# Performance work log

Hardware: AMD Instinct MI355X
Metric: run time of the kernel (lower is better)

## Reference

```python
import jax, jax.numpy as jnp
import numpy as np


def setup_inputs() -> dict:
    key = jax.random.key(0)
    k1, k2 = jax.random.split(key)
    B, N, D = 256, 50000, 2048
    queries = jax.random.normal(k1, (B, D), dtype=jnp.float32)
    bank = jax.random.normal(k2, (N, D), dtype=jnp.float32)
    return {"queries": queries, "bank": bank}


def reference(queries, bank):
    # Cosine similarity of every query against every bank row, fused as one
    # GEMM + row-norm scaling (original repeats the query N times per item
    # in a Python loop; math is identical).
    eps = jnp.float32(1e-12)
    q_norm = jnp.sqrt(jnp.sum(queries * queries, axis=1, keepdims=True))  # [B,1]
    b_norm = jnp.sqrt(jnp.sum(bank * bank, axis=1))                       # [N]
    dots = jnp.einsum('bd,nd->bn', queries, bank)                         # [B,N]
    scores = dots / jnp.maximum(q_norm * b_norm[None, :], eps)
    best_idx = jnp.argmax(scores, axis=1)  # retrieval result per batch item
    return best_idx, scores
```

## Files before the change

### kernel.cpp

```cpp
#include <hip/hip_runtime.h>
#include <stdint.h>

#define MQ 256
#define NB 50000
#define KD 2048
#define BN 64
#define BK 64

typedef __attribute__((ext_vector_type(8))) short bf16x8;
typedef __attribute__((ext_vector_type(4))) float f32x4;

__device__ __forceinline__ unsigned int pack_bf16(float a, float b) {
  unsigned int ua = __float_as_uint(a);
  ua += 0x7fffu + ((ua >> 16) & 1u);
  unsigned int ub = __float_as_uint(b);
  ub += 0x7fffu + ((ub >> 16) & 1u);
  return (ua >> 16) | (ub & 0xffff0000u);
}

__device__ __forceinline__ float wave_sum(float v) {
#pragma unroll
  for (int o = 32; o > 0; o >>= 1) v += __shfl_down(v, o, 64);
  return v;
}
__device__ __forceinline__ float wave_max(float v) {
#pragma unroll
  for (int o = 32; o > 0; o >>= 1) v = fmaxf(v, __shfl_down(v, o, 64));
  return v;
}

__global__ __launch_bounds__(256) void prep_q(const float* __restrict__ q,
                                              unsigned short* __restrict__ qbf,
                                              float* __restrict__ qn) {
  const int b = blockIdx.x, tid = threadIdx.x;
  const float* row = q + (size_t)b * KD;
  float4 v0 = *(const float4*)(row + tid * 8);
  float4 v1 = *(const float4*)(row + tid * 8 + 4);
  float sq = v0.x * v0.x + v0.y * v0.y + v0.z * v0.z + v0.w * v0.w +
             v1.x * v1.x + v1.y * v1.y + v1.z * v1.z + v1.w * v1.w;
  uint4 o;
  o.x = pack_bf16(v0.x, v0.y);
  o.y = pack_bf16(v0.z, v0.w);
  o.z = pack_bf16(v1.x, v1.y);
  o.w = pack_bf16(v1.z, v1.w);
  *(uint4*)(qbf + (size_t)b * KD + tid * 8) = o;
  sq = wave_sum(sq);
  __shared__ float s4[4];
  if ((tid & 63) == 0) s4[tid >> 6] = sq;
  __syncthreads();
  if (tid == 0) qn[b] = sqrtf(s4[0] + s4[1] + s4[2] + s4[3]);
}

__global__ __launch_bounds__(256, 3) void gemm_scores(
    const float* __restrict__ bank, const unsigned short* __restrict__ qbf,
    const float* __restrict__ qn, float* __restrict__ out_scores) {
  __shared__ alignas(16) unsigned short As[MQ * BK];
  __shared__ alignas(16) unsigned short Bs[BN * BK];
  __shared__ float qn_s[MQ];
  __shared__ float bsq_s[256];
  __shared__ float bn_s[BN];

  const int tid = threadIdx.x;
  const int w = tid >> 6;
  const int lane = tid & 63;
  const int n0 = blockIdx.x * BN;

  qn_s[tid] = qn[tid];

  f32x4 acc[4][4] = {};

  const int br = tid >> 2;
  const int bseg = (tid & 3) * 16;
  int brow = n0 + br;
  if (brow >= NB) brow = NB - 1;
  const float* bsrc = bank + (size_t)brow * KD + bseg;

  const int a_row_in_grp = lane >> 3;
  const int a_colb = (lane & 7) * 8;
  float bsq = 0.f;

  for (int kt = 0; kt < KD / BK; ++kt) {
    const int k0 = kt * BK;
#pragma unroll
    for (int i = 0; i < 8; ++i) {
      const int row = w * 64 + i * 8 + a_row_in_grp;
      const unsigned short* src = qbf + (size_t)row * KD + k0 + a_colb;
      unsigned short* dst = &As[row * BK + a_colb];
      __builtin_amdgcn_global_load_lds(
          (const __attribute__((address_space(1))) unsigned int*)src,
          (__attribute__((address_space(3))) unsigned int*)dst, 16, 0, 0);
    }
    float4 f0 = *(const float4*)(bsrc + k0);
    float4 f1 = *(const float4*)(bsrc + k0 + 4);
    float4 f2 = *(const float4*)(bsrc + k0 + 8);
    float4 f3 = *(const float4*)(bsrc + k0 + 12);
    bsq += f0.x * f0.x + f0.y * f0.y + f0.z * f0.z + f0.w * f0.w +
           f1.x * f1.x + f1.y * f1.y + f1.z * f1.z + f1.w * f1.w +
           f2.x * f2.x + f2.y * f2.y + f2.z * f2.z + f2.w * f2.w +
           f3.x * f3.x + f3.y * f3.y + f3.z * f3.z + f3.w * f3.w;
    uint4 w0, w1;
    w0.x = pack_bf16(f0.x, f0.y);
    w0.y = pack_bf16(f0.z, f0.w);
    w0.z = pack_bf16(f1.x, f1.y);
    w0.w = pack_bf16(f1.z, f1.w);
    w1.x = pack_bf16(f2.x, f2.y);
    w1.y = pack_bf16(f2.z, f2.w);
    w1.z = pack_bf16(f3.x, f3.y);
    w1.w = pack_bf16(f3.z, f3.w);
    *(uint4*)&Bs[br * BK + bseg] = w0;
    *(uint4*)&Bs[br * BK + bseg + 8] = w1;
    __syncthreads();
#pragma unroll
    for (int s = 0; s < 2; ++s) {
      bf16x8 af[4], bfv[4];
#pragma unroll
      for (int t = 0; t < 4; ++t) {
        af[t] = *(const bf16x8*)&As[(w * 64 + t * 16 + (lane & 15)) * BK +
                                    s * 32 + (lane >> 4) * 8];
        bfv[t] = *(const bf16x8*)&Bs[(t * 16 + (lane & 15)) * BK + s * 32 +
                                     (lane >> 4) * 8];
      }
#pragma unroll
      for (int tm = 0; tm < 4; ++tm)
#pragma unroll
        for (int tn = 0; tn < 4; ++tn)
          acc[tm][tn] = __builtin_amdgcn_mfma_f32_16x16x32_bf16(
              af[tm], bfv[tn], acc[tm][tn], 0, 0, 0);
    }
    __syncthreads();
  }

  bsq_s[tid] = bsq;
  __syncthreads();
  if (tid < BN)
    bn_s[tid] = sqrtf(bsq_s[tid * 4] + bsq_s[tid * 4 + 1] + bsq_s[tid * 4 + 2] +
                      bsq_s[tid * 4 + 3]);
  __syncthreads();

  const int quad = lane >> 4, nl = lane & 15;
#pragma unroll
  for (int tn = 0; tn < 4; ++tn) {
    const int gn = n0 + tn * 16 + nl;
    if (gn >= NB) continue;
    const float bn = bn_s[tn * 16 + nl];
#pragma unroll
    for (int tm = 0; tm < 4; ++tm) {
#pragma unroll
      for (int r = 0; r < 4; ++r) {
        const int m = w * 64 + tm * 16 + quad * 4 + r;
        const float sc = acc[tm][tn][r] / fmaxf(qn_s[m] * bn, 1e-12f);
        out_scores[(size_t)m * NB + gn] = sc;
      }
    }
  }
}

__global__ __launch_bounds__(256) void argmax_rescue(
    const float* __restrict__ scores, const float* __restrict__ q,
    const float* __restrict__ bank, float* __restrict__ out_idx) {
  const int b = blockIdx.x, tid = threadIdx.x;
  const int w = tid >> 6, lane = tid & 63;
  const float* row = scores + (size_t)b * NB;

  float vmax = -1e30f;
  for (int i = tid; i < NB; i += 256) vmax = fmaxf(vmax, row[i]);
  vmax = wave_max(vmax);
  __shared__ float red[4];
  if (lane == 0) red[w] = vmax;
  __syncthreads();
  const float bmax = fmaxf(fmaxf(red[0], red[1]), fmaxf(red[2], red[3]));
  const float thr = bmax - 2e-3f;

  __shared__ int cand[64];
  __shared__ int cnt;
  if (tid == 0) cnt = 0;
  __syncthreads();
  for (int i = tid; i < NB; i += 256) {
    if (row[i] >= thr) {
      int c = atomicAdd(&cnt, 1);
      if (c < 64) cand[c] = i;
    }
  }
  __syncthreads();
  const int nc = min(cnt, 64);

  __shared__ float dd[4], ss[4];
  float best = -1e30f;
  int bidx = 0x7fffffff;
  const float* qrow = q + (size_t)b * KD;
  for (int c = 0; c < nc; ++c) {
    const int idx = cand[c];
    const float* brow = bank + (size_t)idx * KD;
    float d = 0.f, s = 0.f;
#pragma unroll
    for (int j = 0; j < 8; ++j) {
      const float bv = brow[tid * 8 + j];
      const float qv = qrow[tid * 8 + j];
      d = fmaf(qv, bv, d);
      s = fmaf(bv, bv, s);
    }
    d = wave_sum(d);
    s = wave_sum(s);
    if (lane == 0) {
      dd[w] = d;
      ss[w] = s;
    }
    __syncthreads();
    const float dt = dd[0] + dd[1] + dd[2] + dd[3];
    const float st = ss[0] + ss[1] + ss[2] + ss[3];
    const float sc = dt / fmaxf(sqrtf(st), 1e-12f);
    if (sc > best || (sc == best && idx < bidx)) {
      best = sc;
      bidx = idx;
    }
    __syncthreads();
  }
  if (tid == 0) out_idx[b] = (float)bidx;
}

extern "C" void kernel_launch(void* const* d_in, const int* in_sizes, int n_in,
                              void* d_out, int out_size, void* d_ws,
                              size_t ws_size, hipStream_t stream) {
  const float* queries = (const float*)d_in[0];
  const float* bank = (const float*)d_in[1];
  float* out = (float*)d_out;
  float* out_scores = out + MQ;

  unsigned short* qbf = (unsigned short*)d_ws;
  float* qn = (float*)((char*)d_ws + (size_t)MQ * KD * 2);

  prep_q<<<MQ, 256, 0, stream>>>(queries, qbf, qn);
  gemm_scores<<<(NB + BN - 1) / BN, 256, 0, stream>>>(bank, qbf, qn,
                                                      out_scores);
  argmax_rescue<<<MQ, 256, 0, stream>>>(out_scores, queries, bank, out);
}
```

Measured before the change: 697.1 us.

## Fuse per-block argmax into GEMM epilogue and prefetch bank tiles

```diff
diff --git a/kernel.cpp b/kernel.cpp
--- a/kernel.cpp
+++ b/kernel.cpp
@@ -6,6 +6,8 @@
 #define KD 2048
 #define BN 64
 #define BK 64
+#define KT (KD / BK)
+#define NBLK ((NB + BN - 1) / BN)
 
 typedef __attribute__((ext_vector_type(8))) short bf16x8;
 typedef __attribute__((ext_vector_type(4))) float f32x4;
@@ -18,14 +20,18 @@
   return (ua >> 16) | (ub & 0xffff0000u);
 }
 
+__device__ __forceinline__ unsigned int ordf(float f) {
+  unsigned int u = __float_as_uint(f);
+  return (u & 0x80000000u) ? ~u : (u | 0x80000000u);
+}
+__device__ __forceinline__ float deordf(unsigned int e) {
+  unsigned int u = (e & 0x80000000u) ? (e ^ 0x80000000u) : ~e;
+  return __uint_as_float(u);
+}
+
 __device__ __forceinline__ float wave_sum(float v) {
 #pragma unroll
   for (int o = 32; o > 0; o >>= 1) v += __shfl_down(v, o, 64);
-  return v;
-}
-__device__ __forceinline__ float wave_max(float v) {
-#pragma unroll
-  for (int o = 32; o > 0; o >>= 1) v = fmaxf(v, __shfl_down(v, o, 64));
   return v;
 }
 
@@ -53,7 +59,8 @@
 
 __global__ __launch_bounds__(256, 3) void gemm_scores(
     const float* __restrict__ bank, const unsigned short* __restrict__ qbf,
-    const float* __restrict__ qn, float* __restrict__ out_scores) {
+    const float* __restrict__ qn, float* __restrict__ out_scores,
+    unsigned long long* __restrict__ bm) {
   __shared__ alignas(16) unsigned short As[MQ * BK];
   __shared__ alignas(16) unsigned short Bs[BN * BK];
   __shared__ float qn_s[MQ];
@@ -79,7 +86,12 @@
   const int a_colb = (lane & 7) * 8;
   float bsq = 0.f;
 
-  for (int kt = 0; kt < KD / BK; ++kt) {
+  float4 f0 = *(const float4*)(bsrc);
+  float4 f1 = *(const float4*)(bsrc + 4);
+  float4 f2 = *(const float4*)(bsrc + 8);
+  float4 f3 = *(const float4*)(bsrc + 12);
+
+  for (int kt = 0; kt < KT; ++kt) {
     const int k0 = kt * BK;
 #pragma unroll
     for (int i = 0; i < 8; ++i) {
@@ -90,26 +102,29 @@
           (const __attribute__((address_space(1))) unsigned int*)src,
           (__attribute__((address_space(3))) unsigned int*)dst, 16, 0, 0);
     }
-    float4 f0 = *(const float4*)(bsrc + k0);
-    float4 f1 = *(const float4*)(bsrc + k0 + 4);
-    float4 f2 = *(const float4*)(bsrc + k0 + 8);
-    float4 f3 = *(const float4*)(bsrc + k0 + 12);
     bsq += f0.x * f0.x + f0.y * f0.y + f0.z * f0.z + f0.w * f0.w +
            f1.x * f1.x + f1.y * f1.y + f1.z * f1.z + f1.w * f1.w +
            f2.x * f2.x + f2.y * f2.y + f2.z * f2.z + f2.w * f2.w +
            f3.x * f3.x + f3.y * f3.y + f3.z * f3.z + f3.w * f3.w;
-    uint4 w0, w1;
-    w0.x = pack_bf16(f0.x, f0.y);
-    w0.y = pack_bf16(f0.z, f0.w);
-    w0.z = pack_bf16(f1.x, f1.y);
-    w0.w = pack_bf16(f1.z, f1.w);
-    w1.x = pack_bf16(f2.x, f2.y);
-    w1.y = pack_bf16(f2.z, f2.w);
-    w1.z = pack_bf16(f3.x, f3.y);
-    w1.w = pack_bf16(f3.z, f3.w);
-    *(uint4*)&Bs[br * BK + bseg] = w0;
-    *(uint4*)&Bs[br * BK + bseg + 8] = w1;
-    __syncthreads();
+    uint4 p0, p1;
+    p0.x = pack_bf16(f0.x, f0.y);
+    p0.y = pack_bf16(f0.z, f0.w);
+    p0.z = pack_bf16(f1.x, f1.y);
+    p0.w = pack_bf16(f1.z, f1.w);
+    p1.x = pack_bf16(f2.x, f2.y);
+    p1.y = pack_bf16(f2.z, f2.w);
+    p1.z = pack_bf16(f3.x, f3.y);
+    p1.w = pack_bf16(f3.z, f3.w);
+    *(uint4*)&Bs[br * BK + bseg] = p0;
+    *(uint4*)&Bs[br * BK + bseg + 8] = p1;
+    __syncthreads();
+    if (kt + 1 < KT) {
+      const float* p = bsrc + (kt + 1) * BK;
+      f0 = *(const float4*)(p);
+      f1 = *(const float4*)(p + 4);
+      f2 = *(const float4*)(p + 8);
+      f3 = *(const float4*)(p + 12);
+    }
 #pragma unroll
     for (int s = 0; s < 2; ++s) {
       bf16x8 af[4], bfv[4];
@@ -139,46 +154,76 @@
 
   const int quad = lane >> 4, nl = lane & 15;
 #pragma unroll
-  for (int tn = 0; tn < 4; ++tn) {
-    const int gn = n0 + tn * 16 + nl;
-    if (gn >= NB) continue;
-    const float bn = bn_s[tn * 16 + nl];
-#pragma unroll
-    for (int tm = 0; tm < 4; ++tm) {
-#pragma unroll
-      for (int r = 0; r < 4; ++r) {
-        const int m = w * 64 + tm * 16 + quad * 4 + r;
-        const float sc = acc[tm][tn][r] / fmaxf(qn_s[m] * bn, 1e-12f);
-        out_scores[(size_t)m * NB + gn] = sc;
-      }
+  for (int tm = 0; tm < 4; ++tm) {
+#pragma unroll
+    for (int r = 0; r < 4; ++r) {
+      const int m = w * 64 + tm * 16 + quad * 4 + r;
+      const float qm = qn_s[m];
+      unsigned long long best = 0ull;
+#pragma unroll
+      for (int tn = 0; tn < 4; ++tn) {
+        const int gn = n0 + tn * 16 + nl;
+        if (gn < NB) {
+          const float sc =
+              acc[tm][tn][r] / fmaxf(qm * bn_s[tn * 16 + nl], 1e-12f);
+          out_scores[(size_t)m * NB + gn] = sc;
+          const unsigned long long pk =
+              ((unsigned long long)ordf(sc) << 32) | (unsigned int)gn;
+          best = pk > best ? pk : best;
+        }
+      }
+#pragma unroll
+      for (int mask = 1; mask < 16; mask <<= 1) {
+        const unsigned long long o = __shfl_xor(best, mask, 64);
+        best = o > best ? o : best;
+      }
+      if (nl == 0) bm[(size_t)m * NBLK + blockIdx.x] = best;
     }
   }
 }
 
 __global__ __launch_bounds__(256) void argmax_rescue(
-    const float* __restrict__ scores, const float* __restrict__ q,
-    const float* __restrict__ bank, float* __restrict__ out_idx) {
+    const unsigned long long* __restrict__ bm, const float* __restrict__ scores,
+    const float* __restrict__ q, const float* __restrict__ bank,
+    float* __restrict__ out_idx) {
   const int b = blockIdx.x, tid = threadIdx.x;
   const int w = tid >> 6, lane = tid & 63;
-  const float* row = scores + (size_t)b * NB;
-
-  float vmax = -1e30f;
-  for (int i = tid; i < NB; i += 256) vmax = fmaxf(vmax, row[i]);
-  vmax = wave_max(vmax);
-  __shared__ float red[4];
-  if (lane == 0) red[w] = vmax;
-  __syncthreads();
-  const float bmax = fmaxf(fmaxf(red[0], red[1]), fmaxf(red[2], red[3]));
-  const float thr = bmax - 2e-3f;
+  const unsigned long long* rbm = bm + (size_t)b * NBLK;
+
+  unsigned long long pmax = 0ull;
+  for (int i = tid; i < NBLK; i += 256) {
+    const unsigned long long v = rbm[i];
+    pmax = v > pmax ? v : pmax;
+  }
+#pragma unroll
+  for (int o = 32; o > 0; o >>= 1) {
+    const unsigned long long v = __shfl_down(pmax, o, 64);
+    pmax = v > pmax ? v : pmax;
+  }
+  __shared__ unsigned long long red[4];
+  if (lane == 0) red[w] = pmax;
+  __syncthreads();
+  unsigned long long gmax = red[0];
+#pragma unroll
+  for (int i = 1; i < 4; ++i) gmax = red[i] > gmax ? red[i] : gmax;
+  const float thr = deordf((unsigned int)(gmax >> 32)) - 2e-3f;
 
   __shared__ int cand[64];
   __shared__ int cnt;
   if (tid == 0) cnt = 0;
   __syncthreads();
-  for (int i = tid; i < NB; i += 256) {
-    if (row[i] >= thr) {
-      int c = atomicAdd(&cnt, 1);
-      if (c < 64) cand[c] = i;
+  const float* srow = scores + (size_t)b * NB;
+  for (int i = tid; i < NBLK; i += 256) {
+    const float bmf = deordf((unsigned int)(rbm[i] >> 32));
+    if (bmf >= thr) {
+      const int base = i * BN;
+      const int lim = min(BN, NB - base);
+      for (int j = 0; j < lim; ++j) {
+        if (srow[base + j] >= thr) {
+          const int c = atomicAdd(&cnt, 1);
+          if (c < 64) cand[c] = base + j;
+        }
+      }
     }
   }
   __syncthreads();
@@ -226,11 +271,13 @@
   float* out = (float*)d_out;
   float* out_scores = out + MQ;
 
-  unsigned short* qbf = (unsigned short*)d_ws;
-  float* qn = (float*)((char*)d_ws + (size_t)MQ * KD * 2);
+  char* ws = (char*)d_ws;
+  unsigned short* qbf = (unsigned short*)ws;
+  float* qn = (float*)(ws + (size_t)MQ * KD * 2);
+  unsigned long long* bm =
+      (unsigned long long*)(ws + (size_t)MQ * KD * 2 + 2048);
 
   prep_q<<<MQ, 256, 0, stream>>>(queries, qbf, qn);
-  gemm_scores<<<(NB + BN - 1) / BN, 256, 0, stream>>>(bank, qbf, qn,
-                                                      out_scores);
-  argmax_rescue<<<MQ, 256, 0, stream>>>(out_scores, queries, bank, out);
-}
+  gemm_scores<<<NBLK, 256, 0, stream>>>(bank, qbf, qn, out_scores, bm);
+  argmax_rescue<<<MQ, 256, 0, stream>>>(bm, out_scores, queries, bank, out);
+}
```

New measurement: 641.7 us. 1.09x faster.
